# Performance work log

Measured on AMD Instinct MI355X. Metric: run time of the kernel, lower is better.

Reference implementation:

```python
import jax, jax.numpy as jnp
import numpy as np

S = 7          # grid size
C = 10         # num classes (SVHN digits)
L_COORD = 5.0
L_NOOBJ = 0.5
EPS = 1e-6     # safe-sqrt epsilon (original sqrt(clamp(x,0,1)) has inf grad at 0)


def _iou(b1, b2):
    """Vectorized translation of computeIOU. b1, b2: [..., 4] as (left, top, w, h)."""
    l1l, l1t, w1, h1 = b1[..., 0], b1[..., 1], b1[..., 2], b1[..., 3]
    l2l, l2t, w2, h2 = b2[..., 0], b2[..., 1], b2[..., 2], b2[..., 3]
    l1r, l1b = l1l + w1, l1t + h1
    l2r, l2b = l2l + w2, l2t + h2
    a1 = w1 * h1
    a2 = w2 * h2
    cont_by2 = (l2l <= l1l) & (l2t <= l1t) & (l2r >= l1r) & (l2b >= l1b)  # box2 contains box1
    cont_by1 = (l1l <= l2l) & (l1t <= l2t) & (l1r >= l2r) & (l1b >= l2b)  # box1 contains box2
    sep = (l1r <= l2l) | (l2r <= l1l) | (l1b <= l2t) | (l2b <= l1t)       # disjoint
    iw = jnp.minimum(l1r, l2r) - jnp.maximum(l1l, l2l)
    ih = jnp.minimum(l1b, l2b) - jnp.maximum(l1t, l2t)
    inter = iw * ih
    gen = inter / (a1 + a2 - inter)
    return jnp.where(cont_by2, a1 / a2,
           jnp.where(cont_by1, a2 / a1,
           jnp.where(sep, jnp.zeros_like(gen), gen)))


def setup_inputs() -> dict:
    key = jax.random.key(0)
    k1, k2, k3, k4 = jax.random.split(key, 4)
    N = 16384
    pred_tensor = jax.random.normal(k1, (N, S, S, 20), dtype=jnp.float32)
    xywh = jax.random.uniform(k2, (N, S, S, 4), dtype=jnp.float32)
    conf = (jax.random.uniform(k3, (N, S, S, 1)) < 0.15).astype(jnp.float32)  # ~7 objects/img
    cls = jax.random.randint(k4, (N, S, S, 1), 0, C).astype(jnp.float32)
    target_tensor = jnp.concatenate([xywh, conf, cls], axis=-1)
    return {"pred_tensor": pred_tensor, "target_tensor": target_tensor}


def reference(pred_tensor, target_tensor):
    N = pred_tensor.shape[0]
    conf_t = target_tensor[..., 4]                       # [N,S,S]
    coo = (conf_t > 0).astype(pred_tensor.dtype)
    noo = (conf_t == 0).astype(pred_tensor.dtype)

    # no-object confidence loss: both predicted confidences vs target conf (=0 on noo cells)
    noobj_loss = jnp.sum(noo * ((pred_tensor[..., 4] - conf_t) ** 2 +
                                (pred_tensor[..., 9] - conf_t) ** 2))

    # responsible-box selection via IoU (vectorized replacement of the python loop)
    bt = target_tensor[..., :4]                          # target box [N,S,S,4]
    bp0 = pred_tensor[..., 0:5]
    bp1 = pred_tensor[..., 5:10]
    iou0 = _iou(bp0[..., :4], bt)
    iou1 = _iou(bp1[..., :4], bt)
    pick0 = iou0 >= iou1                                 # box0 responsible when tie or higher
    max_iou = jax.lax.stop_gradient(jnp.where(pick0, iou0, iou1))  # Variable() detach in orig
    resp = jnp.where(pick0[..., None], bp0, bp1)         # responsible pred box [N,S,S,5]
    nonresp = jnp.where(pick0[..., None], bp1, bp0)

    contain_loss = jnp.sum(coo * (resp[..., 4] - max_iou) ** 2)

    xy_p = jnp.clip(resp[..., :2], 0.0, 1.0)
    xy_t = jnp.clip(bt[..., :2], 0.0, 1.0)
    wh_p = jnp.sqrt(jnp.clip(resp[..., 2:4], EPS, 1.0))
    wh_t = jnp.sqrt(jnp.clip(bt[..., 2:4], EPS, 1.0))
    loc_loss = jnp.sum(coo[..., None] * ((xy_p - xy_t) ** 2 + (wh_p - wh_t) ** 2))

    not_contain_loss = jnp.sum(coo * nonresp[..., 4] ** 2)  # target conf forced to 0

    # class cross-entropy (sum reduction) over object cells
    logits = pred_tensor[..., 10:]                       # [N,S,S,10]
    logz = jax.nn.logsumexp(logits, axis=-1)
    cls_idx = target_tensor[..., 5].astype(jnp.int32)
    picked = jnp.take_along_axis(logits, cls_idx[..., None], axis=-1)[..., 0]
    class_loss = jnp.sum(coo * (logz - picked))

    total = (L_COORD * loc_loss + 2.0 * contain_loss + not_contain_loss +
             L_NOOBJ * noobj_loss + class_loss)
    return total / N
```

## Files before the change

kernel.cpp:

```cpp
#include <hip/hip_runtime.h>


#define SBLK 256

constexpr float L_COORD = 5.0f;
constexpr float L_NOOBJ = 0.5f;
constexpr float EPS_    = 1e-6f;

typedef __attribute__((address_space(3))) uint32_t lds_u32_t;
typedef const __attribute__((address_space(1))) uint32_t glb_u32_t;

__device__ __forceinline__ float clamp01(float x) { return fminf(fmaxf(x, 0.0f), 1.0f); }

__device__ __forceinline__ float iou_f(float l1l, float l1t, float w1, float h1,
                                       float l2l, float l2t, float w2, float h2) {
    float l1r = l1l + w1, l1b = l1t + h1;
    float l2r = l2l + w2, l2b = l2t + h2;
    float a1 = w1 * h1, a2 = w2 * h2;
    bool cont_by2 = (l2l <= l1l) && (l2t <= l1t) && (l2r >= l1r) && (l2b >= l1b);
    bool cont_by1 = (l1l <= l2l) && (l1t <= l2t) && (l1r >= l2r) && (l1b >= l2b);
    bool sep = (l1r <= l2l) || (l2r <= l1l) || (l1b <= l2t) || (l2b <= l1t);
    float iw = fminf(l1r, l2r) - fmaxf(l1l, l2l);
    float ih = fminf(l1b, l2b) - fmaxf(l1t, l2t);
    float inter = iw * ih;
    float gen = inter * __builtin_amdgcn_rcpf(a1 + a2 - inter);
    float r = sep ? 0.0f : gen;
    r = cont_by1 ? a2 * __builtin_amdgcn_rcpf(a1) : r;
    r = cont_by2 ? a1 * __builtin_amdgcn_rcpf(a2) : r;
    return r;
}

__global__ __launch_bounds__(SBLK) void yolo_loss_kernel(
        const float* __restrict__ pred, const float* __restrict__ tgt,
        double* __restrict__ partials, int ncells) {
    __shared__ float4 sp4[SBLK * 5];
    int block0 = blockIdx.x * SBLK;
    int i = block0 + threadIdx.x;

    const float4* pg = reinterpret_cast<const float4*>(pred) + (size_t)block0 * 5;
    int nf4 = (ncells - block0) * 5;
    #pragma unroll
    for (int k = 0; k < 5; ++k) {
        int j = threadIdx.x + k * SBLK;
        if (j < nf4) {
            __builtin_amdgcn_global_load_lds((glb_u32_t*)(pg + j),
                                             (lds_u32_t*)(&sp4[j]), 16, 0, 0);
        }
    }

    float2 t0, t1, tc;
    if (i < ncells) {
        const float2* tg = reinterpret_cast<const float2*>(tgt) + (size_t)i * 3;
        t0 = tg[0]; t1 = tg[1]; tc = tg[2];
    } else {
        t0 = t1 = tc = make_float2(0.f, 0.f);
    }
    __syncthreads();

    float total = 0.0f;
    if (i < ncells) {
        float4 pa = sp4[threadIdx.x * 5 + 0];
        float4 pb = sp4[threadIdx.x * 5 + 1];
        float4 pc = sp4[threadIdx.x * 5 + 2];
        float4 pd = sp4[threadIdx.x * 5 + 3];
        float4 pe = sp4[threadIdx.x * 5 + 4];

        float conf = tc.x;
        float coo = (conf > 0.0f) ? 1.0f : 0.0f;
        float noo = (conf == 0.0f) ? 1.0f : 0.0f;

        float d0 = pb.x - conf, d1 = pc.y - conf;
        float noobj = noo * (d0 * d0 + d1 * d1);

        float b0l = pa.x, b0t = pa.y, b0w = pa.z, b0h = pa.w, b0c = pb.x;
        float b1l = pb.y, b1t = pb.z, b1w = pb.w, b1h = pc.x, b1c = pc.y;
        float btl = t0.x, btt = t0.y, btw = t1.x, bth = t1.y;

        float iou0 = iou_f(b0l, b0t, b0w, b0h, btl, btt, btw, bth);
        float iou1 = iou_f(b1l, b1t, b1w, b1h, btl, btt, btw, bth);
        bool pick0 = (iou0 >= iou1);
        float max_iou = pick0 ? iou0 : iou1;

        float rl = pick0 ? b0l : b1l;
        float rt = pick0 ? b0t : b1t;
        float rw = pick0 ? b0w : b1w;
        float rh = pick0 ? b0h : b1h;
        float rc = pick0 ? b0c : b1c;
        float nc = pick0 ? b1c : b0c;

        float cd = rc - max_iou;
        float contain = cd * cd;
        float not_contain = nc * nc;

        float ex = clamp01(rl) - clamp01(btl);
        float ey = clamp01(rt) - clamp01(btt);
        float sw = __builtin_amdgcn_sqrtf(fminf(fmaxf(rw, EPS_), 1.0f))
                 - __builtin_amdgcn_sqrtf(fminf(fmaxf(btw, EPS_), 1.0f));
        float sh = __builtin_amdgcn_sqrtf(fminf(fmaxf(rh, EPS_), 1.0f))
                 - __builtin_amdgcn_sqrtf(fminf(fmaxf(bth, EPS_), 1.0f));
        float loc = ex * ex + ey * ey + sw * sw + sh * sh;

        float lg0 = pc.z, lg1 = pc.w;
        float lg2 = pd.x, lg3 = pd.y, lg4 = pd.z, lg5 = pd.w;
        float lg6 = pe.x, lg7 = pe.y, lg8 = pe.z, lg9 = pe.w;
        float m = fmaxf(lg0, lg1);
        m = fmaxf(m, fmaxf(lg2, lg3));
        m = fmaxf(m, fmaxf(lg4, lg5));
        m = fmaxf(m, fmaxf(lg6, lg7));
        m = fmaxf(m, fmaxf(lg8, lg9));
        float ssum = __expf(lg0 - m) + __expf(lg1 - m) + __expf(lg2 - m) +
                     __expf(lg3 - m) + __expf(lg4 - m) + __expf(lg5 - m) +
                     __expf(lg6 - m) + __expf(lg7 - m) + __expf(lg8 - m) +
                     __expf(lg9 - m);
        float logz = m + __logf(ssum);
        int ci = (int)tc.y;
        float picked = lg0;
        picked = (ci == 1) ? lg1 : picked;
        picked = (ci == 2) ? lg2 : picked;
        picked = (ci == 3) ? lg3 : picked;
        picked = (ci == 4) ? lg4 : picked;
        picked = (ci == 5) ? lg5 : picked;
        picked = (ci == 6) ? lg6 : picked;
        picked = (ci == 7) ? lg7 : picked;
        picked = (ci == 8) ? lg8 : picked;
        picked = (ci == 9) ? lg9 : picked;
        float cls_loss = logz - picked;

        total = L_COORD * (coo * loc)
              + 2.0f * (coo * contain)
              + (coo * not_contain)
              + L_NOOBJ * noobj
              + coo * cls_loss;
    }

    float v = total;
    #pragma unroll
    for (int off = 32; off > 0; off >>= 1)
        v += __shfl_down(v, off, 64);
    __shared__ float smw[SBLK / 64];
    int lane = threadIdx.x & 63;
    int wid  = threadIdx.x >> 6;
    if (lane == 0) smw[wid] = v;
    __syncthreads();
    if (threadIdx.x == 0) {
        double s = 0.0;
        #pragma unroll
        for (int w = 0; w < SBLK / 64; ++w) s += (double)smw[w];
        partials[blockIdx.x] = s;
    }
}

#define RBLK 1024

__global__ __launch_bounds__(RBLK) void yolo_reduce_kernel(
        const double* __restrict__ partials, int nparts,
        float* __restrict__ out, double invN) {
    double v = 0.0;
    for (int idx = threadIdx.x; idx < nparts; idx += RBLK)
        v += partials[idx];
    #pragma unroll
    for (int off = 32; off > 0; off >>= 1)
        v += __shfl_down(v, off, 64);
    __shared__ double sm[RBLK / 64];
    int lane = threadIdx.x & 63;
    int wid  = threadIdx.x >> 6;
    if (lane == 0) sm[wid] = v;
    __syncthreads();
    if (threadIdx.x == 0) {
        double s = 0.0;
        #pragma unroll
        for (int w = 0; w < RBLK / 64; ++w) s += sm[w];
        out[0] = (float)(s * invN);
    }
}

extern "C" void kernel_launch(void* const* d_in, const int* in_sizes, int n_in,
                              void* d_out, int out_size, void* d_ws, size_t ws_size,
                              hipStream_t stream) {
    const float* pred = (const float*)d_in[0];
    const float* tgt  = (const float*)d_in[1];
    int ncells = in_sizes[0] / 20;
    int N = ncells / 49;

    int nblocks = (ncells + SBLK - 1) / SBLK;
    yolo_loss_kernel<<<nblocks, SBLK, 0, stream>>>(pred, tgt, (double*)d_ws, ncells);
    yolo_reduce_kernel<<<1, RBLK, 0, stream>>>((const double*)d_ws, nblocks,
                                               (float*)d_out, 1.0 / (double)N);
}
```

Baseline: 22.20 us.

## Fuse final reduction via last-block ticket and process four cells per thread

```diff
diff --git a/kernel.cpp b/kernel.cpp
--- a/kernel.cpp
+++ b/kernel.cpp
@@ -2,13 +2,12 @@
 
 
 #define SBLK 256
+#define CPT  4
+#define CPB  (SBLK * CPT)
 
 constexpr float L_COORD = 5.0f;
 constexpr float L_NOOBJ = 0.5f;
 constexpr float EPS_    = 1e-6f;
-
-typedef __attribute__((address_space(3))) uint32_t lds_u32_t;
-typedef const __attribute__((address_space(1))) uint32_t glb_u32_t;
 
 __device__ __forceinline__ float clamp01(float x) { return fminf(fmaxf(x, 0.0f), 1.0f); }
 
@@ -30,114 +29,114 @@
     return r;
 }
 
-__global__ __launch_bounds__(SBLK) void yolo_loss_kernel(
+__device__ __forceinline__ float cell_loss(float4 pa, float4 pb, float4 pc,
+                                           float4 pd, float4 pe,
+                                           float2 t0, float2 t1, float2 tc) {
+    float conf = tc.x;
+    float coo = (conf > 0.0f) ? 1.0f : 0.0f;
+    float noo = (conf == 0.0f) ? 1.0f : 0.0f;
+
+    float d0 = pb.x - conf, d1 = pc.y - conf;
+    float noobj = noo * (d0 * d0 + d1 * d1);
+
+    float b0l = pa.x, b0t = pa.y, b0w = pa.z, b0h = pa.w, b0c = pb.x;
+    float b1l = pb.y, b1t = pb.z, b1w = pb.w, b1h = pc.x, b1c = pc.y;
+    float btl = t0.x, btt = t0.y, btw = t1.x, bth = t1.y;
+
+    float iou0 = iou_f(b0l, b0t, b0w, b0h, btl, btt, btw, bth);
+    float iou1 = iou_f(b1l, b1t, b1w, b1h, btl, btt, btw, bth);
+    bool pick0 = (iou0 >= iou1);
+    float max_iou = pick0 ? iou0 : iou1;
+
+    float rl = pick0 ? b0l : b1l;
+    float rt = pick0 ? b0t : b1t;
+    float rw = pick0 ? b0w : b1w;
+    float rh = pick0 ? b0h : b1h;
+    float rc = pick0 ? b0c : b1c;
+    float nc = pick0 ? b1c : b0c;
+
+    float cd = rc - max_iou;
+    float contain = cd * cd;
+    float not_contain = nc * nc;
+
+    float ex = clamp01(rl) - clamp01(btl);
+    float ey = clamp01(rt) - clamp01(btt);
+    float sw = __builtin_amdgcn_sqrtf(fminf(fmaxf(rw, EPS_), 1.0f))
+             - __builtin_amdgcn_sqrtf(fminf(fmaxf(btw, EPS_), 1.0f));
+    float sh = __builtin_amdgcn_sqrtf(fminf(fmaxf(rh, EPS_), 1.0f))
+             - __builtin_amdgcn_sqrtf(fminf(fmaxf(bth, EPS_), 1.0f));
+    float loc = ex * ex + ey * ey + sw * sw + sh * sh;
+
+    float lg0 = pc.z, lg1 = pc.w;
+    float lg2 = pd.x, lg3 = pd.y, lg4 = pd.z, lg5 = pd.w;
+    float lg6 = pe.x, lg7 = pe.y, lg8 = pe.z, lg9 = pe.w;
+    float m = fmaxf(lg0, lg1);
+    m = fmaxf(m, fmaxf(lg2, lg3));
+    m = fmaxf(m, fmaxf(lg4, lg5));
+    m = fmaxf(m, fmaxf(lg6, lg7));
+    m = fmaxf(m, fmaxf(lg8, lg9));
+    float ssum = __expf(lg0 - m) + __expf(lg1 - m) + __expf(lg2 - m) +
+                 __expf(lg3 - m) + __expf(lg4 - m) + __expf(lg5 - m) +
+                 __expf(lg6 - m) + __expf(lg7 - m) + __expf(lg8 - m) +
+                 __expf(lg9 - m);
+    float logz = m + __logf(ssum);
+    int ci = (int)tc.y;
+    float picked = lg0;
+    picked = (ci == 1) ? lg1 : picked;
+    picked = (ci == 2) ? lg2 : picked;
+    picked = (ci == 3) ? lg3 : picked;
+    picked = (ci == 4) ? lg4 : picked;
+    picked = (ci == 5) ? lg5 : picked;
+    picked = (ci == 6) ? lg6 : picked;
+    picked = (ci == 7) ? lg7 : picked;
+    picked = (ci == 8) ? lg8 : picked;
+    picked = (ci == 9) ? lg9 : picked;
+    float cls_loss = logz - picked;
+
+    return L_COORD * (coo * loc)
+         + 2.0f * (coo * contain)
+         + (coo * not_contain)
+         + L_NOOBJ * noobj
+         + coo * cls_loss;
+}
+
+__global__ __launch_bounds__(SBLK) void yolo_loss_fused(
         const float* __restrict__ pred, const float* __restrict__ tgt,
-        double* __restrict__ partials, int ncells) {
-    __shared__ float4 sp4[SBLK * 5];
-    int block0 = blockIdx.x * SBLK;
-    int i = block0 + threadIdx.x;
+        double* __restrict__ partials, unsigned* __restrict__ ticket,
+        float* __restrict__ out, int ncells, double invN) {
+    __shared__ float smw[SBLK / 64];
+    __shared__ double smd[SBLK / 64];
+    __shared__ int last_flag;
 
-    const float4* pg = reinterpret_cast<const float4*>(pred) + (size_t)block0 * 5;
-    int nf4 = (ncells - block0) * 5;
+    int block0 = blockIdx.x * CPB;
+    int nblocks = gridDim.x;
+
+    float4 pa[CPT], pb[CPT], pc[CPT], pd[CPT], pe[CPT];
+    float2 t0[CPT], t1[CPT], tc[CPT];
     #pragma unroll
-    for (int k = 0; k < 5; ++k) {
-        int j = threadIdx.x + k * SBLK;
-        if (j < nf4) {
-            __builtin_amdgcn_global_load_lds((glb_u32_t*)(pg + j),
-                                             (lds_u32_t*)(&sp4[j]), 16, 0, 0);
+    for (int k = 0; k < CPT; ++k) {
+        int ik = block0 + k * SBLK + threadIdx.x;
+        if (ik < ncells) {
+            const float4* p4 = reinterpret_cast<const float4*>(pred + (size_t)ik * 20);
+            pa[k] = p4[0]; pb[k] = p4[1]; pc[k] = p4[2]; pd[k] = p4[3]; pe[k] = p4[4];
+            const float2* t2 = reinterpret_cast<const float2*>(tgt + (size_t)ik * 6);
+            t0[k] = t2[0]; t1[k] = t2[1]; tc[k] = t2[2];
+        } else {
+            pa[k] = pb[k] = pc[k] = pd[k] = pe[k] = make_float4(0.f, 0.f, 0.f, 0.f);
+            t0[k] = t1[k] = make_float2(0.f, 0.f);
+            tc[k] = make_float2(-1.0f, 0.f);
         }
     }
 
-    float2 t0, t1, tc;
-    if (i < ncells) {
-        const float2* tg = reinterpret_cast<const float2*>(tgt) + (size_t)i * 3;
-        t0 = tg[0]; t1 = tg[1]; tc = tg[2];
-    } else {
-        t0 = t1 = tc = make_float2(0.f, 0.f);
-    }
-    __syncthreads();
-
     float total = 0.0f;
-    if (i < ncells) {
-        float4 pa = sp4[threadIdx.x * 5 + 0];
-        float4 pb = sp4[threadIdx.x * 5 + 1];
-        float4 pc = sp4[threadIdx.x * 5 + 2];
-        float4 pd = sp4[threadIdx.x * 5 + 3];
-        float4 pe = sp4[threadIdx.x * 5 + 4];
-
-        float conf = tc.x;
-        float coo = (conf > 0.0f) ? 1.0f : 0.0f;
-        float noo = (conf == 0.0f) ? 1.0f : 0.0f;
-
-        float d0 = pb.x - conf, d1 = pc.y - conf;
-        float noobj = noo * (d0 * d0 + d1 * d1);
-
-        float b0l = pa.x, b0t = pa.y, b0w = pa.z, b0h = pa.w, b0c = pb.x;
-        float b1l = pb.y, b1t = pb.z, b1w = pb.w, b1h = pc.x, b1c = pc.y;
-        float btl = t0.x, btt = t0.y, btw = t1.x, bth = t1.y;
-
-        float iou0 = iou_f(b0l, b0t, b0w, b0h, btl, btt, btw, bth);
-        float iou1 = iou_f(b1l, b1t, b1w, b1h, btl, btt, btw, bth);
-        bool pick0 = (iou0 >= iou1);
-        float max_iou = pick0 ? iou0 : iou1;
-
-        float rl = pick0 ? b0l : b1l;
-        float rt = pick0 ? b0t : b1t;
-        float rw = pick0 ? b0w : b1w;
-        float rh = pick0 ? b0h : b1h;
-        float rc = pick0 ? b0c : b1c;
-        float nc = pick0 ? b1c : b0c;
-
-        float cd = rc - max_iou;
-        float contain = cd * cd;
-        float not_contain = nc * nc;
-
-        float ex = clamp01(rl) - clamp01(btl);
-        float ey = clamp01(rt) - clamp01(btt);
-        float sw = __builtin_amdgcn_sqrtf(fminf(fmaxf(rw, EPS_), 1.0f))
-                 - __builtin_amdgcn_sqrtf(fminf(fmaxf(btw, EPS_), 1.0f));
-        float sh = __builtin_amdgcn_sqrtf(fminf(fmaxf(rh, EPS_), 1.0f))
-                 - __builtin_amdgcn_sqrtf(fminf(fmaxf(bth, EPS_), 1.0f));
-        float loc = ex * ex + ey * ey + sw * sw + sh * sh;
-
-        float lg0 = pc.z, lg1 = pc.w;
-        float lg2 = pd.x, lg3 = pd.y, lg4 = pd.z, lg5 = pd.w;
-        float lg6 = pe.x, lg7 = pe.y, lg8 = pe.z, lg9 = pe.w;
-        float m = fmaxf(lg0, lg1);
-        m = fmaxf(m, fmaxf(lg2, lg3));
-        m = fmaxf(m, fmaxf(lg4, lg5));
-        m = fmaxf(m, fmaxf(lg6, lg7));
-        m = fmaxf(m, fmaxf(lg8, lg9));
-        float ssum = __expf(lg0 - m) + __expf(lg1 - m) + __expf(lg2 - m) +
-                     __expf(lg3 - m) + __expf(lg4 - m) + __expf(lg5 - m) +
-                     __expf(lg6 - m) + __expf(lg7 - m) + __expf(lg8 - m) +
-                     __expf(lg9 - m);
-        float logz = m + __logf(ssum);
-        int ci = (int)tc.y;
-        float picked = lg0;
-        picked = (ci == 1) ? lg1 : picked;
-        picked = (ci == 2) ? lg2 : picked;
-        picked = (ci == 3) ? lg3 : picked;
-        picked = (ci == 4) ? lg4 : picked;
-        picked = (ci == 5) ? lg5 : picked;
-        picked = (ci == 6) ? lg6 : picked;
-        picked = (ci == 7) ? lg7 : picked;
-        picked = (ci == 8) ? lg8 : picked;
-        picked = (ci == 9) ? lg9 : picked;
-        float cls_loss = logz - picked;
-
-        total = L_COORD * (coo * loc)
-              + 2.0f * (coo * contain)
-              + (coo * not_contain)
-              + L_NOOBJ * noobj
-              + coo * cls_loss;
-    }
+    #pragma unroll
+    for (int k = 0; k < CPT; ++k)
+        total += cell_loss(pa[k], pb[k], pc[k], pd[k], pe[k], t0[k], t1[k], tc[k]);
 
     float v = total;
     #pragma unroll
     for (int off = 32; off > 0; off >>= 1)
         v += __shfl_down(v, off, 64);
-    __shared__ float smw[SBLK / 64];
     int lane = threadIdx.x & 63;
     int wid  = threadIdx.x >> 6;
     if (lane == 0) smw[wid] = v;
@@ -147,30 +146,29 @@
         #pragma unroll
         for (int w = 0; w < SBLK / 64; ++w) s += (double)smw[w];
         partials[blockIdx.x] = s;
+        __threadfence();
+        unsigned prev = atomicAdd(ticket, 1u);
+        last_flag = (prev == (unsigned)(nblocks - 1)) ? 1 : 0;
     }
-}
+    __syncthreads();
 
-#define RBLK 1024
-
-__global__ __launch_bounds__(RBLK) void yolo_reduce_kernel(
-        const double* __restrict__ partials, int nparts,
-        float* __restrict__ out, double invN) {
-    double v = 0.0;
-    for (int idx = threadIdx.x; idx < nparts; idx += RBLK)
-        v += partials[idx];
-    #pragma unroll
-    for (int off = 32; off > 0; off >>= 1)
-        v += __shfl_down(v, off, 64);
-    __shared__ double sm[RBLK / 64];
-    int lane = threadIdx.x & 63;
-    int wid  = threadIdx.x >> 6;
-    if (lane == 0) sm[wid] = v;
-    __syncthreads();
-    if (threadIdx.x == 0) {
+    if (last_flag) {
+        __threadfence();
         double s = 0.0;
+        for (int idx = threadIdx.x; idx < nblocks; idx += SBLK)
+            s += __hip_atomic_load(&partials[idx], __ATOMIC_RELAXED,
+                                   __HIP_MEMORY_SCOPE_AGENT);
         #pragma unroll
-        for (int w = 0; w < RBLK / 64; ++w) s += sm[w];
-        out[0] = (float)(s * invN);
+        for (int off = 32; off > 0; off >>= 1)
+            s += __shfl_down(s, off, 64);
+        if (lane == 0) smd[wid] = s;
+        __syncthreads();
+        if (threadIdx.x == 0) {
+            double t = 0.0;
+            #pragma unroll
+            for (int w = 0; w < SBLK / 64; ++w) t += smd[w];
+            out[0] = (float)(t * invN);
+        }
     }
 }
 
@@ -182,8 +180,12 @@
     int ncells = in_sizes[0] / 20;
     int N = ncells / 49;
 
-    int nblocks = (ncells + SBLK - 1) / SBLK;
-    yolo_loss_kernel<<<nblocks, SBLK, 0, stream>>>(pred, tgt, (double*)d_ws, ncells);
-    yolo_reduce_kernel<<<1, RBLK, 0, stream>>>((const double*)d_ws, nblocks,
-                                               (float*)d_out, 1.0 / (double)N);
+    int nblocks = (ncells + CPB - 1) / CPB;
+    double* partials = (double*)d_ws;
+    unsigned* ticket = (unsigned*)((char*)d_ws + (size_t)nblocks * sizeof(double));
+
+    hipMemsetAsync(ticket, 0, sizeof(unsigned), stream);
+    yolo_loss_fused<<<nblocks, SBLK, 0, stream>>>(pred, tgt, partials, ticket,
+                                                  (float*)d_out, ncells,
+                                                  1.0 / (double)N);
 }
```

Measured after the change: 49.41 us. 123% more time.
